# Optimization experiments

Measured on AMD Instinct MI355X. Metric: run time of the kernel, lower is better.

The kernel has to match this reference:

```python
import jax, jax.numpy as jnp
import numpy as np

MANT_BITS = 8  # static quantize_param_dict values for Positional_0/1/2
_PWL_X = jnp.linspace(-4.0, 4.0, 33, dtype=jnp.float32)
_PWL_Y = 0.5 * _PWL_X * (1.0 + jax.lax.erf(_PWL_X / jnp.sqrt(jnp.float32(2.0))))


def float2fix(x, mantissa_bits):
    """Fixed-point quantization: round to multiples of 2^-mantissa_bits (STE grad)."""
    s = jnp.float32(2.0 ** mantissa_bits)
    q = jnp.round(x * s) / s
    return x + jax.lax.stop_gradient(q - x)


def pwlin_gelu_basic(x, mantissa_bits_in, mantissa_bits_out):
    """Piecewise-linear GELU: quantized input, linear interp of exact GELU on
    [-4,4] (33 breakpoints), 0 for x<-4, identity for x>4, quantized output."""
    xq = float2fix(x, mantissa_bits_in)
    y = jnp.interp(xq, _PWL_X, _PWL_Y)
    y = jnp.where(xq > 4.0, xq, jnp.where(xq < -4.0, jnp.float32(0.0), y))
    return float2fix(y, mantissa_bits_out)


def setup_inputs() -> dict:
    key = jax.random.key(0)
    k_x, k_w1, k_b1, k_w2, k_b2 = jax.random.split(key, 5)
    dim, ff_dim = 1024, 4096
    B, S = 32, 512
    sc1 = 1.0 / np.sqrt(dim)
    sc2 = 1.0 / np.sqrt(ff_dim)
    return {
        "x": jax.random.normal(k_x, (B, S, dim), dtype=jnp.float32),
        "w1": jax.random.uniform(k_w1, (dim, ff_dim), jnp.float32, -sc1, sc1),
        "b1": jax.random.uniform(k_b1, (ff_dim,), jnp.float32, -sc1, sc1),
        "w2": jax.random.uniform(k_w2, (ff_dim, dim), jnp.float32, -sc2, sc2),
        "b2": jax.random.uniform(k_b2, (dim,), jnp.float32, -sc2, sc2),
    }


def reference(x, w1, b1, w2, b2):
    # fc1 GEMM + quantize epilogue
    h = jnp.einsum("bsd,df->bsf", x, w1) + b1          # [B,S,ff_dim]
    h = float2fix(h, MANT_BITS)                         # Positional_0
    # piecewise-linear GELU with quantized in/out
    h = pwlin_gelu_basic(h, MANT_BITS, MANT_BITS)
    h = float2fix(h, MANT_BITS)                         # Positional_1
    # fc2 GEMM + quantize epilogue
    out = jnp.einsum("bsf,fd->bsd", h, w2) + b2         # [B,S,dim]
    return float2fix(out, MANT_BITS)                    # Positional_2
```

## Files before the change

### kernel.cpp

```cpp
#include <hip/hip_runtime.h>
#include <hip/hip_bf16.h>

typedef __bf16 bf16_t;
typedef __bf16 bf16x8 __attribute__((ext_vector_type(8)));
typedef __bf16 bf16x4 __attribute__((ext_vector_type(4)));
typedef float f32x4 __attribute__((ext_vector_type(4)));

#define QS   256.0f
#define QINV 0.00390625f

__device__ __forceinline__ void async_copy16(const bf16_t* g, bf16_t* l) {
  __builtin_amdgcn_global_load_lds(
      (__attribute__((address_space(1))) void*)g,
      (__attribute__((address_space(3))) void*)l,
      16, 0, 0);
}

template <bool GELU, typename OutT, bool XSWZ>
__global__ __launch_bounds__(256, 4)
void gemm_tile(const bf16_t* __restrict__ A, const bf16_t* __restrict__ Bt,
               const float* __restrict__ bias, OutT* __restrict__ C,
               int M, int N, int K) {
  __shared__ __attribute__((aligned(16))) bf16_t As[128 * 64];
  __shared__ __attribute__((aligned(16))) bf16_t Bs[128 * 64];

  const int tid = threadIdx.x;
  const int lane = tid & 63;
  const int wv = tid >> 6;
  const int wy = wv >> 1;
  const int wx = wv & 1;
  const int l15 = lane & 15;
  const int lq = lane >> 4;

  float ytA = 0.f, ytS = 0.f;
  if (GELU) {
    float xv = -4.0f + 0.25f * (float)lane;
    float y0 = 0.5f * xv * (1.0f + erff(xv * 0.70710678f));
    float xv1 = xv + 0.25f;
    float y1 = 0.5f * xv1 * (1.0f + erff(xv1 * 0.70710678f));
    ytA = y0;
    ytS = y1 - y0;
  }

  int bx = blockIdx.x, by = blockIdx.y;
  if (XSWZ) {
    const int gx = gridDim.x;
    const int nwg = gx * gridDim.y;
    const int f = by * gx + bx;
    const int chunk = nwg >> 3;
    const int f2 = (f & 7) * chunk + (f >> 3);
    bx = f2 % gx;
    by = f2 / gx;
  }

  const int mBase = by * 128;
  const int nBase = bx * 128;

  const bf16_t* aTile = A + (size_t)mBase * K;
  const bf16_t* bTile = Bt + (size_t)nBase * K;

  f32x4 acc[4][4];
#pragma unroll
  for (int i = 0; i < 4; ++i)
#pragma unroll
    for (int j = 0; j < 4; ++j)
      acc[i][j] = (f32x4){0.f, 0.f, 0.f, 0.f};

  const int srow = tid >> 3;
  const int scb = (((tid & 7) ^ ((tid >> 3) & 7)) * 8);

  const int swz_r = l15 & 7;

  for (int k0 = 0; k0 < K; k0 += 64) {
#pragma unroll
    for (int p = 0; p < 4; ++p) {
      const int row = p * 32 + srow;
      const size_t go = (size_t)row * K + k0 + scb;
      const int lo = (p * 256 + wv * 64) * 8;
      async_copy16(aTile + go, As + lo);
      async_copy16(bTile + go, Bs + lo);
    }
    __syncthreads();

#pragma unroll
    for (int ks = 0; ks < 2; ++ks) {
      const int swzA = ((ks * 4 + lq) ^ swz_r) * 8;
      bf16x8 af[4], bfr[4];
#pragma unroll
      for (int i = 0; i < 4; ++i) {
        af[i]  = *(const bf16x8*)(As + (wy * 64 + i * 16 + l15) * 64 + swzA);
        bfr[i] = *(const bf16x8*)(Bs + (wx * 64 + i * 16 + l15) * 64 + swzA);
      }
#pragma unroll
      for (int i = 0; i < 4; ++i)
#pragma unroll
        for (int j = 0; j < 4; ++j)
          acc[i][j] = __builtin_amdgcn_mfma_f32_16x16x32_bf16(af[i], bfr[j], acc[i][j], 0, 0, 0);
    }
    __syncthreads();
  }

  float bj[4];
#pragma unroll
  for (int j = 0; j < 4; ++j)
    bj[j] = bias[nBase + wx * 64 + j * 16 + l15];

#pragma unroll
  for (int i = 0; i < 4; ++i) {
    const int rb = mBase + wy * 64 + i * 16 + lq * 4;
#pragma unroll
    for (int j = 0; j < 4; ++j) {
      const int cn = nBase + wx * 64 + j * 16 + l15;
#pragma unroll
      for (int r = 0; r < 4; ++r) {
        float c = acc[i][j][r] + bj[j];
        float v;
        if (GELU) {
          float xq = rintf(c * QS) * QINV;
          float t = (xq + 4.0f) * 4.0f;
          int ii = (int)t;
          ii = ii < 0 ? 0 : (ii > 31 ? 31 : ii);
          float f = t - (float)ii;
          float y0 = __shfl(ytA, ii);
          float sl = __shfl(ytS, ii);
          v = fmaf(f, sl, y0);
          v = (xq > 4.0f) ? xq : v;
          v = (xq < -4.0f) ? 0.0f : v;
          v = rintf(v * QS) * QINV;
        } else {
          v = rintf(c * QS) * QINV;
        }
        C[(size_t)(rb + r) * N + cn] = (OutT)v;
      }
    }
  }
}

__global__ __launch_bounds__(256)
void prep_kernel(const float* __restrict__ x, bf16_t* __restrict__ xb,
                 const float* __restrict__ w1, bf16_t* __restrict__ w1t,
                 const float* __restrict__ w2, bf16_t* __restrict__ w2t) {
  __shared__ float t[32][33];
  const int id = blockIdx.x;
  const int tid = threadIdx.x;
  if (id < 16384) {
    const int idx = id * 256 + tid;
    const float4 v = ((const float4*)x)[idx];
    bf16x4 o;
    o[0] = (bf16_t)v.x; o[1] = (bf16_t)v.y; o[2] = (bf16_t)v.z; o[3] = (bf16_t)v.w;
    ((bf16x4*)xb)[idx] = o;
  } else {
    const float* in; bf16_t* out; int R, C, bx, by;
    if (id < 20480) {
      const int id2 = id - 16384;
      in = w1; out = w1t; R = 1024; C = 4096;
      bx = id2 & 127; by = id2 >> 7;
    } else {
      const int id3 = id - 20480;
      in = w2; out = w2t; R = 4096; C = 1024;
      bx = id3 & 31; by = id3 >> 5;
    }
    const int c0 = bx * 32;
    const int r0 = by * 32;
    const int tx = tid & 31;
    const int ty = tid >> 5;
#pragma unroll
    for (int dy = 0; dy < 32; dy += 8)
      t[ty + dy][tx] = in[(size_t)(r0 + ty + dy) * C + c0 + tx];
    __syncthreads();
#pragma unroll
    for (int dy = 0; dy < 32; dy += 8)
      out[(size_t)(c0 + ty + dy) * R + r0 + tx] = (bf16_t)t[tx][ty + dy];
  }
}

extern "C" void kernel_launch(void* const* d_in, const int* in_sizes, int n_in,
                              void* d_out, int out_size, void* d_ws, size_t ws_size,
                              hipStream_t stream) {
  const float* x  = (const float*)d_in[0];
  const float* w1 = (const float*)d_in[1];
  const float* b1 = (const float*)d_in[2];
  const float* w2 = (const float*)d_in[3];
  const float* b2 = (const float*)d_in[4];
  float* out = (float*)d_out;

  const int M = 16384, D = 1024, F = 4096;

  char* ws = (char*)d_ws;
  size_t off = 0;
  bf16_t* xb  = (bf16_t*)(ws + off); off += (size_t)M * D * 2;
  bf16_t* w1t = (bf16_t*)(ws + off); off += (size_t)D * F * 2;
  bf16_t* w2t = (bf16_t*)(ws + off); off += (size_t)F * D * 2;
  bf16_t* h   = (bf16_t*)(ws + off);

  prep_kernel<<<16384 + 4096 + 4096, 256, 0, stream>>>(x, xb, w1, w1t, w2, w2t);

  gemm_tile<true, bf16_t, true><<<dim3(F / 128, M / 128), 256, 0, stream>>>(xb, w1t, b1, h, M, F, D);
  gemm_tile<false, float, true><<<dim3(D / 128, M / 128), 256, 0, stream>>>(h, w2t, b2, out, M, D, F);
}
```

Before: 430.1 us.

## Switch GEMM inner loop to 32x32x16 MFMA with 2x2 per-wave tiles

New measurement: 447.9 us. 4.1% more time.

```diff
diff --git a/kernel.cpp b/kernel.cpp
--- a/kernel.cpp
+++ b/kernel.cpp
@@ -4,7 +4,7 @@
 typedef __bf16 bf16_t;
 typedef __bf16 bf16x8 __attribute__((ext_vector_type(8)));
 typedef __bf16 bf16x4 __attribute__((ext_vector_type(4)));
-typedef float f32x4 __attribute__((ext_vector_type(4)));
+typedef float f32x16 __attribute__((ext_vector_type(16)));
 
 #define QS   256.0f
 #define QINV 0.00390625f
@@ -17,7 +17,7 @@
 }
 
 template <bool GELU, typename OutT, bool XSWZ>
-__global__ __launch_bounds__(256, 4)
+__global__ __launch_bounds__(256, 3)
 void gemm_tile(const bf16_t* __restrict__ A, const bf16_t* __restrict__ Bt,
                const float* __restrict__ bias, OutT* __restrict__ C,
                int M, int N, int K) {
@@ -29,8 +29,8 @@
   const int wv = tid >> 6;
   const int wy = wv >> 1;
   const int wx = wv & 1;
-  const int l15 = lane & 15;
-  const int lq = lane >> 4;
+  const int l31 = lane & 31;
+  const int lh = lane >> 5;
 
   float ytA = 0.f, ytS = 0.f;
   if (GELU) {
@@ -59,17 +59,20 @@
   const bf16_t* aTile = A + (size_t)mBase * K;
   const bf16_t* bTile = Bt + (size_t)nBase * K;
 
-  f32x4 acc[4][4];
-#pragma unroll
-  for (int i = 0; i < 4; ++i)
-#pragma unroll
-    for (int j = 0; j < 4; ++j)
-      acc[i][j] = (f32x4){0.f, 0.f, 0.f, 0.f};
+  f32x16 acc[2][2];
+#pragma unroll
+  for (int i = 0; i < 2; ++i)
+#pragma unroll
+    for (int j = 0; j < 2; ++j)
+      acc[i][j] = (f32x16){0.f, 0.f, 0.f, 0.f, 0.f, 0.f, 0.f, 0.f,
+                           0.f, 0.f, 0.f, 0.f, 0.f, 0.f, 0.f, 0.f};
 
   const int srow = tid >> 3;
   const int scb = (((tid & 7) ^ ((tid >> 3) & 7)) * 8);
 
-  const int swz_r = l15 & 7;
+  const int r7 = l31 & 7;
+  const int baseA = (wy * 64 + l31) * 64;
+  const int baseB = (wx * 64 + l31) * 64;
 
   for (int k0 = 0; k0 < K; k0 += 64) {
 #pragma unroll
@@ -83,37 +86,37 @@
     __syncthreads();
 
 #pragma unroll
-    for (int ks = 0; ks < 2; ++ks) {
-      const int swzA = ((ks * 4 + lq) ^ swz_r) * 8;
-      bf16x8 af[4], bfr[4];
-#pragma unroll
-      for (int i = 0; i < 4; ++i) {
-        af[i]  = *(const bf16x8*)(As + (wy * 64 + i * 16 + l15) * 64 + swzA);
-        bfr[i] = *(const bf16x8*)(Bs + (wx * 64 + i * 16 + l15) * 64 + swzA);
+    for (int ks = 0; ks < 4; ++ks) {
+      const int phys = ((ks * 2 + lh) ^ r7) * 8;
+      bf16x8 af[2], bfr[2];
+#pragma unroll
+      for (int i = 0; i < 2; ++i) {
+        af[i]  = *(const bf16x8*)(As + baseA + i * 32 * 64 + phys);
+        bfr[i] = *(const bf16x8*)(Bs + baseB + i * 32 * 64 + phys);
       }
 #pragma unroll
-      for (int i = 0; i < 4; ++i)
-#pragma unroll
-        for (int j = 0; j < 4; ++j)
-          acc[i][j] = __builtin_amdgcn_mfma_f32_16x16x32_bf16(af[i], bfr[j], acc[i][j], 0, 0, 0);
+      for (int i = 0; i < 2; ++i)
+#pragma unroll
+        for (int j = 0; j < 2; ++j)
+          acc[i][j] = __builtin_amdgcn_mfma_f32_32x32x16_bf16(af[i], bfr[j], acc[i][j], 0, 0, 0);
     }
     __syncthreads();
   }
 
-  float bj[4];
-#pragma unroll
-  for (int j = 0; j < 4; ++j)
-    bj[j] = bias[nBase + wx * 64 + j * 16 + l15];
-
-#pragma unroll
-  for (int i = 0; i < 4; ++i) {
-    const int rb = mBase + wy * 64 + i * 16 + lq * 4;
-#pragma unroll
-    for (int j = 0; j < 4; ++j) {
-      const int cn = nBase + wx * 64 + j * 16 + l15;
-#pragma unroll
-      for (int r = 0; r < 4; ++r) {
-        float c = acc[i][j][r] + bj[j];
+  float bj[2];
+#pragma unroll
+  for (int j = 0; j < 2; ++j)
+    bj[j] = bias[nBase + wx * 64 + j * 32 + l31];
+
+#pragma unroll
+  for (int i = 0; i < 2; ++i) {
+#pragma unroll
+    for (int j = 0; j < 2; ++j) {
+      const int cn = nBase + wx * 64 + j * 32 + l31;
+#pragma unroll
+      for (int reg = 0; reg < 16; ++reg) {
+        const int rm = mBase + wy * 64 + i * 32 + (reg & 3) + 8 * (reg >> 2) + 4 * lh;
+        float c = acc[i][j][reg] + bj[j];
         float v;
         if (GELU) {
           float xq = rintf(c * QS) * QINV;
@@ -130,7 +133,7 @@
         } else {
           v = rintf(c * QS) * QINV;
         }
-        C[(size_t)(rb + r) * N + cn] = (OutT)v;
+        C[(size_t)rm * N + cn] = (OutT)v;
       }
     }
   }
@@ -195,6 +198,6 @@
 
   prep_kernel<<<16384 + 4096 + 4096, 256, 0, stream>>>(x, xb, w1, w1t, w2, w2t);
 
-  gemm_tile<true, bf16_t, true><<<dim3(F / 128, M / 128), 256, 0, stream>>>(xb, w1t, b1, h, M, F, D);
+  gemm_tile<true, bf16_t, false><<<dim3(F / 128, M / 128), 256, 0, stream>>>(xb, w1t, b1, h, M, F, D);
   gemm_tile<false, float, true><<<dim3(D / 128, M / 128), 256, 0, stream>>>(h, w2t, b2, out, M, D, F);
 }
```
